# Performance work log

Hardware: AMD Instinct MI355X
Metric: run time of the kernel (lower is better)

The kernel has to match this reference:

```python
import jax, jax.numpy as jnp
import numpy as np

N_NODES = 10000
N_RAND_EDGES = 320000
IN_DIM = 256
HIDDEN = 64
HEADS = 8
OUT_DIM = 256
NEG_SLOPE = 0.2


def setup_inputs() -> dict:
    key = jax.random.key(0)
    ks = jax.random.split(key, 9)
    h = jax.random.normal(ks[0], (N_NODES, IN_DIM), dtype=jnp.float32)
    # random edges + self-loops so every dst has >=1 incoming edge
    src = jnp.concatenate([
        jax.random.randint(ks[1], (N_RAND_EDGES,), 0, N_NODES, dtype=jnp.int32),
        jnp.arange(N_NODES, dtype=jnp.int32)])
    dst = jnp.concatenate([
        jax.random.randint(ks[2], (N_RAND_EDGES,), 0, N_NODES, dtype=jnp.int32),
        jnp.arange(N_NODES, dtype=jnp.int32)])
    def glorot(k, shape):
        fan = shape[0] + shape[-1]
        s = jnp.sqrt(2.0 / fan).astype(jnp.float32)
        return jax.random.normal(k, shape, dtype=jnp.float32) * s
    W1 = glorot(ks[3], (IN_DIM, HEADS * HIDDEN))
    attn_l1 = glorot(ks[4], (HEADS, HIDDEN))
    attn_r1 = glorot(ks[5], (HEADS, HIDDEN))
    W2 = glorot(ks[6], (HEADS * HIDDEN, OUT_DIM))
    attn_l2 = glorot(ks[7], (1, OUT_DIM))
    attn_r2 = glorot(ks[8], (1, OUT_DIM))
    return {"h": h, "W1": W1, "attn_l1": attn_l1, "attn_r1": attn_r1,
            "W2": W2, "attn_l2": attn_l2, "attn_r2": attn_r2,
            "src": src, "dst": dst}


def gat_conv(x, W, attn_l, attn_r, src, dst, n_nodes):
    # x: [N, F_in]; W: [F_in, H*D]; attn_l/attn_r: [H, D]
    H, D = attn_l.shape
    feat = (x @ W).reshape(n_nodes, H, D)          # [N, H, D]
    el = jnp.einsum('nhd,hd->nh', feat, attn_l)    # [N, H]
    er = jnp.einsum('nhd,hd->nh', feat, attn_r)
    e = jax.nn.leaky_relu(el[src] + er[dst], NEG_SLOPE)  # [E, H]
    # edge softmax over incoming edges of each destination node
    m = jax.ops.segment_max(e, dst, num_segments=n_nodes)      # [N, H]
    ex = jnp.exp(e - m[dst])                                   # [E, H]
    denom = jax.ops.segment_sum(ex, dst, num_segments=n_nodes) # [N, H]
    alpha = ex / denom[dst]                                    # [E, H]
    out = jax.ops.segment_sum(alpha[:, :, None] * feat[src], dst,
                              num_segments=n_nodes)            # [N, H, D]
    return out.reshape(n_nodes, H * D)


def reference(h, W1, attn_l1, attn_r1, W2, attn_l2, attn_r2, src, dst):
    n = h.shape[0]
    x = gat_conv(h, W1, attn_l1, attn_r1, src, dst, n)   # [N, H*hidden]
    x = jax.nn.elu(x)
    out = gat_conv(x, W2, attn_l2, attn_r2, src, dst, n) # [N, out_dim]
    return out
```

## Files before the change

### kernel.cpp

```cpp
#include <hip/hip_runtime.h>
#include <hip/hip_bf16.h>

#define N_NODES 10000
#define IN_DIM 256
#define HID 512
#define HEADS 8
#define OUT_DIM 256
#define NEG 0.2f
#define CAP 128
#define WT_BLOCKS 64

typedef __hip_bfloat16 bf16;
typedef __attribute__((ext_vector_type(8))) short short8;
typedef __attribute__((ext_vector_type(4))) float f32x4;

__device__ __forceinline__ float ldm(const void* p, long i, int mode){
  if(mode) return ((const float*)p)[i];
  return __bfloat162float(((const bf16*)p)[i]);
}
__device__ __forceinline__ unsigned short f2bf(float f){
  bf16 b = __float2bfloat16(f);
  return *(unsigned short*)&b;
}
__device__ __forceinline__ float bflo(unsigned int u){ return __uint_as_float(u<<16); }
__device__ __forceinline__ float bfhi(unsigned int u){ return __uint_as_float(u&0xffff0000u); }

__global__ void detect_zero_k(const unsigned short* w1raw, int* mode, int* cnt,
                              float* el2, float* er2){
  int t = threadIdx.x;
  if(blockIdx.x==0){
    __shared__ int sbad;
    if(t==0) sbad=0;
    __syncthreads();
    int bad=0;
    for(int i=t;i<512;i+=256){
      unsigned int u = ((unsigned int)w1raw[i])<<16;
      float f = __uint_as_float(u);
      if(!(f==f) || fabsf(f) > 100.0f) bad++;
    }
    #pragma unroll
    for(int o=32;o>0;o>>=1) bad += __shfl_down(bad,o);
    if((t&63)==0) atomicAdd(&sbad, bad);
    __syncthreads();
    if(t==0) *mode = (sbad>10) ? 1 : 0;
  } else {
    int i = (blockIdx.x-1)*256 + t;
    if(i<N_NODES){ cnt[i]=0; el2[i]=0.f; er2[i]=0.f; }
  }
}

__global__ void prep2_k(const void* W1, const void* W2, unsigned short* wt1,
                        unsigned short* wt2, const int* modep,
                        const int* src, const int* dst, int* cnt, int* bucket, int E){
  int b = blockIdx.x, t = threadIdx.x;
  if(b < WT_BLOCKS){
    int md = *modep;
    __shared__ __align__(16) unsigned short tl[64*72];
    int isW2 = (b>=32);
    int bb = isW2 ? b-32 : b;
    const void* W = isW2 ? W2 : W1;
    unsigned short* wt = isW2 ? wt2 : wt1;
    int K = isW2 ? HID : IN_DIM;
    int N = isW2 ? OUT_DIM : HID;
    int sh = isW2 ? 2 : 3;
    int kt = bb >> sh, nt = bb & ((1<<sh)-1);
    int r = t>>2, c0 = (t&3)<<4;
    long srow = (long)(kt*64 + r)*N + nt*64 + c0;
    unsigned short v[16] __attribute__((aligned(16)));
    if(md){
      const float* Wf = (const float*)W;
      #pragma unroll
      for(int j=0;j<16;j+=4){
        float4 xv = *(const float4*)(Wf + srow + j);
        v[j]=f2bf(xv.x); v[j+1]=f2bf(xv.y); v[j+2]=f2bf(xv.z); v[j+3]=f2bf(xv.w);
      }
    } else {
      const unsigned short* Wb = (const unsigned short*)W;
      *(short8*)&v[0] = *(const short8*)(Wb+srow);
      *(short8*)&v[8] = *(const short8*)(Wb+srow+8);
    }
    #pragma unroll
    for(int j=0;j<16;j++) tl[(c0+j)*72 + r] = v[j];
    __syncthreads();
    int nn = t>>2, k0 = (t&3)<<4;
    short8 o0 = *(short8*)&tl[nn*72+k0];
    short8 o1 = *(short8*)&tl[nn*72+k0+8];
    long drow = (long)(nt*64+nn)*K + kt*64 + k0;
    *(short8*)(wt+drow)   = o0;
    *(short8*)(wt+drow+8) = o1;
  } else {
    int e = (b-WT_BLOCKS)*256 + t;
    if(e<E){
      int d = dst[e];
      int pos = atomicAdd(&cnt[d], 1);
      if(pos < CAP) bucket[(long)d*CAP + pos] = src[e];
    }
  }
}

__global__ __launch_bounds__(256) void gemm_k(const void* A, const unsigned short* Bt,
                                              unsigned short* C, int M, int N, int K,
                                              int asel, const int* modep,
                                              const void* al, const void* ar,
                                              float* el, float* er, int dmode){
  int md = *modep;
  int am = asel ? md : 0;
  __shared__ short As[64*40];
  __shared__ short Bs[64*40];
  __shared__ float led[64], ler[64];
  int t = threadIdx.x;
  int lane = t & 63, wave = t >> 6;
  int l15 = lane & 15, quad = lane >> 4;
  int wm = (wave>>1)*32, wn = (wave&1)*32;
  int mbase = blockIdx.y*64, nbase = blockIdx.x*64;

  f32x4 acc[2][2];
  #pragma unroll
  for(int i=0;i<2;i++)
    #pragma unroll
    for(int j=0;j<2;j++) acc[i][j] = (f32x4){0.f,0.f,0.f,0.f};

  int row = t>>2, kk = (t&3)*8;
  long arow = (long)(mbase+row)*K, brow = (long)(nbase+row)*K;
  bool av = (mbase+row) < M;
  const unsigned short* Ab = (const unsigned short*)A;
  const float* Af = (const float*)A;

  for(int k0=0;k0<K;k0+=32){
    short8 a = (short8){0,0,0,0,0,0,0,0};
    if(am){
      if(av){
        float4 x = *(const float4*)(Af + arow + k0 + kk);
        float4 y = *(const float4*)(Af + arow + k0 + kk + 4);
        a[0]=f2bf(x.x); a[1]=f2bf(x.y); a[2]=f2bf(x.z); a[3]=f2bf(x.w);
        a[4]=f2bf(y.x); a[5]=f2bf(y.y); a[6]=f2bf(y.z); a[7]=f2bf(y.w);
      }
    } else {
      if(av) a = *(const short8*)(Ab + arow + k0 + kk);
    }
    short8 b = *(const short8*)(Bt + brow + k0 + kk);
    __syncthreads();
    *(short8*)(As + row*40 + kk) = a;
    *(short8*)(Bs + row*40 + kk) = b;
    __syncthreads();
    short8 af[2], bfr[2];
    #pragma unroll
    for(int mi=0;mi<2;mi++) af[mi]  = *(short8*)(As + (wm + mi*16 + l15)*40 + quad*8);
    #pragma unroll
    for(int ni=0;ni<2;ni++) bfr[ni] = *(short8*)(Bs + (wn + ni*16 + l15)*40 + quad*8);
    #pragma unroll
    for(int mi=0;mi<2;mi++)
      #pragma unroll
      for(int ni=0;ni<2;ni++)
        acc[mi][ni] = __builtin_amdgcn_mfma_f32_16x16x32_bf16(af[mi], bfr[ni], acc[mi][ni], 0,0,0);
  }

  #pragma unroll
  for(int mi=0;mi<2;mi++){
    #pragma unroll
    for(int ni=0;ni<2;ni++){
      int grow0 = mbase + wm + mi*16 + quad*4;
      int gcol  = nbase + wn + ni*16 + l15;
      #pragma unroll
      for(int r=0;r<4;r++){
        int grow = grow0 + r;
        if(grow < M) C[(long)grow*N + gcol] = f2bf(acc[mi][ni][r]);
      }
    }
  }

  float avv[2], rvv[2];
  #pragma unroll
  for(int ni=0;ni<2;ni++){
    int gc = nbase + wn + ni*16 + l15;
    avv[ni] = ldm(al, gc, md);
    rvv[ni] = ldm(ar, gc, md);
  }
  __syncthreads();
  if(t<64){ led[t]=0.f; ler[t]=0.f; }
  __syncthreads();
  #pragma unroll
  for(int mi=0;mi<2;mi++){
    #pragma unroll
    for(int r=0;r<4;r++){
      float pl = acc[mi][0][r]*avv[0] + acc[mi][1][r]*avv[1];
      float pr = acc[mi][0][r]*rvv[0] + acc[mi][1][r]*rvv[1];
      #pragma unroll
      for(int o=1;o<16;o<<=1){ pl += __shfl_xor(pl,o); pr += __shfl_xor(pr,o); }
      if(l15==0){
        int lr = wm + mi*16 + quad*4 + r;
        atomicAdd(&led[lr], pl);
        atomicAdd(&ler[lr], pr);
      }
    }
  }
  __syncthreads();
  if(t<64){
    int grow = mbase + t;
    if(grow < M){
      if(dmode==1){
        el[(long)grow*HEADS + blockIdx.x] = led[t];
        er[(long)grow*HEADS + blockIdx.x] = ler[t];
      } else {
        atomicAdd(&el[grow], led[t]);
        atomicAdd(&er[grow], ler[t]);
      }
    }
  }
}

__global__ __launch_bounds__(128) void agg1_k(const unsigned short* fb, const float* el,
                       const float* er, const int* cnt, const int* bucket, unsigned short* x){
  int n = blockIdx.x;
  int t = threadIdx.x;
  long off = (long)n*CAP;
  int deg = cnt[n]; if(deg>CAP) deg=CAP;
  __shared__ int sidx[CAP];
  __shared__ __align__(16) float swl[CAP*8];
  __shared__ float pws[2][8];
  __shared__ float sinv[8];
  __shared__ __align__(16) float pacc[64][8];
  for(int i=t;i<deg;i+=128) sidx[i]=bucket[off+i];
  __syncthreads();
  const float* erp = er + (long)n*HEADS;
  float4 era = *(const float4*)erp, erb = *(const float4*)(erp+4);
  float err8[8] = {era.x,era.y,era.z,era.w,erb.x,erb.y,erb.z,erb.w};
  float pw[8];
  #pragma unroll
  for(int j=0;j<8;j++) pw[j]=0.f;
  for(int i=t;i<deg;i+=128){
    int s = sidx[i];
    const float* ep = el + (long)s*HEADS;
    float4 ea = *(const float4*)ep, eb = *(const float4*)(ep+4);
    float ev[8] = {ea.x,ea.y,ea.z,ea.w,eb.x,eb.y,eb.z,eb.w};
    float wv[8];
    #pragma unroll
    for(int j=0;j<8;j++){
      float e = ev[j] + err8[j];
      e = e>0.f ? e : NEG*e;
      float w = __expf(e);
      wv[j]=w; pw[j]+=w;
    }
    *(float4*)&swl[i*8]   = make_float4(wv[0],wv[1],wv[2],wv[3]);
    *(float4*)&swl[i*8+4] = make_float4(wv[4],wv[5],wv[6],wv[7]);
  }
  #pragma unroll
  for(int o=32;o>0;o>>=1)
    #pragma unroll
    for(int j=0;j<8;j++) pw[j]+=__shfl_xor(pw[j],o);
  int wv_ = t>>6, l = t&63;
  if(l==0){
    #pragma unroll
    for(int j=0;j<8;j++) pws[wv_][j]=pw[j];
  }
  __syncthreads();
  if(t<8){ float s2 = pws[0][t]+pws[1][t]; sinv[t] = s2>0.f ? 1.f/s2 : 0.f; }
  __syncthreads();
  int h = l>>3;
  int c0 = 8*l;
  float a0=0.f,a1=0.f,a2=0.f,a3=0.f,a4=0.f,a5=0.f,a6=0.f,a7=0.f;
  #pragma unroll 4
  for(int i=wv_; i<deg; i+=2){
    int s = sidx[i];
    float w = swl[i*8+h];
    uint4 u = *(const uint4*)(fb + (long)s*HID + c0);
    a0 += w*bflo(u.x); a1 += w*bfhi(u.x);
    a2 += w*bflo(u.y); a3 += w*bfhi(u.y);
    a4 += w*bflo(u.z); a5 += w*bfhi(u.z);
    a6 += w*bflo(u.w); a7 += w*bfhi(u.w);
  }
  if(wv_==1){
    *(float4*)&pacc[l][0] = make_float4(a0,a1,a2,a3);
    *(float4*)&pacc[l][4] = make_float4(a4,a5,a6,a7);
  }
  __syncthreads();
  if(wv_==0){
    float4 q0 = *(float4*)&pacc[l][0], q1 = *(float4*)&pacc[l][4];
    a0+=q0.x; a1+=q0.y; a2+=q0.z; a3+=q0.w;
    a4+=q1.x; a5+=q1.y; a6+=q1.z; a7+=q1.w;
    float inv = sinv[h];
    a0*=inv; a1*=inv; a2*=inv; a3*=inv; a4*=inv; a5*=inv; a6*=inv; a7*=inv;
    a0 = a0>0.f ? a0 : __expf(a0)-1.f;
    a1 = a1>0.f ? a1 : __expf(a1)-1.f;
    a2 = a2>0.f ? a2 : __expf(a2)-1.f;
    a3 = a3>0.f ? a3 : __expf(a3)-1.f;
    a4 = a4>0.f ? a4 : __expf(a4)-1.f;
    a5 = a5>0.f ? a5 : __expf(a5)-1.f;
    a6 = a6>0.f ? a6 : __expf(a6)-1.f;
    a7 = a7>0.f ? a7 : __expf(a7)-1.f;
    uint4 o4;
    o4.x = (unsigned int)f2bf(a0) | ((unsigned int)f2bf(a1)<<16);
    o4.y = (unsigned int)f2bf(a2) | ((unsigned int)f2bf(a3)<<16);
    o4.z = (unsigned int)f2bf(a4) | ((unsigned int)f2bf(a5)<<16);
    o4.w = (unsigned int)f2bf(a6) | ((unsigned int)f2bf(a7)<<16);
    *(uint4*)(x + (long)n*HID + c0) = o4;
  }
}

__global__ __launch_bounds__(64) void agg2_k(const unsigned short* fb, const float* el,
                       const float* er, const int* cnt, const int* bucket, void* out,
                       const int* modep){
  int md = *modep;
  int n = blockIdx.x, t = threadIdx.x;
  long off = (long)n*CAP;
  int deg = cnt[n]; if(deg>CAP) deg=CAP;
  __shared__ int sidx[CAP];
  __shared__ float wl[CAP];
  for(int i=t;i<deg;i+=64) sidx[i]=bucket[off+i];
  __syncthreads();
  float ern = er[n];
  float pw = 0.f;
  for(int i=t;i<deg;i+=64){
    int s = sidx[i];
    float e = el[s]+ern; e = e>0.f ? e : NEG*e;
    float w = __expf(e);
    wl[i]=w;
    pw += w;
  }
  #pragma unroll
  for(int o=32;o>0;o>>=1) pw += __shfl_xor(pw,o);
  float inv = pw>0.f ? 1.f/pw : 0.f;
  __syncthreads();
  int half = t>>5, l = t&31;
  int c0 = 8*l;
  float a0=0.f,a1=0.f,a2=0.f,a3=0.f,a4=0.f,a5=0.f,a6=0.f,a7=0.f;
  #pragma unroll 4
  for(int i=half; i<deg; i+=2){
    int s = sidx[i];
    float w = wl[i];
    uint4 u = *(const uint4*)(fb + (long)s*OUT_DIM + c0);
    a0 += w*bflo(u.x); a1 += w*bfhi(u.x);
    a2 += w*bflo(u.y); a3 += w*bfhi(u.y);
    a4 += w*bflo(u.z); a5 += w*bfhi(u.z);
    a6 += w*bflo(u.w); a7 += w*bfhi(u.w);
  }
  a0 += __shfl_xor(a0,32); a1 += __shfl_xor(a1,32);
  a2 += __shfl_xor(a2,32); a3 += __shfl_xor(a3,32);
  a4 += __shfl_xor(a4,32); a5 += __shfl_xor(a5,32);
  a6 += __shfl_xor(a6,32); a7 += __shfl_xor(a7,32);
  if(half==0){
    a0*=inv; a1*=inv; a2*=inv; a3*=inv; a4*=inv; a5*=inv; a6*=inv; a7*=inv;
    long oi = (long)n*OUT_DIM + c0;
    if(md){
      float* of = (float*)out;
      *(float4*)(of+oi)   = make_float4(a0,a1,a2,a3);
      *(float4*)(of+oi+4) = make_float4(a4,a5,a6,a7);
    } else {
      unsigned short* ob = (unsigned short*)out;
      uint4 o4;
      o4.x = (unsigned int)f2bf(a0) | ((unsigned int)f2bf(a1)<<16);
      o4.y = (unsigned int)f2bf(a2) | ((unsigned int)f2bf(a3)<<16);
      o4.z = (unsigned int)f2bf(a4) | ((unsigned int)f2bf(a5)<<16);
      o4.w = (unsigned int)f2bf(a6) | ((unsigned int)f2bf(a7)<<16);
      *(uint4*)(ob+oi) = o4;
    }
  }
}

extern "C" void kernel_launch(void* const* d_in, const int* in_sizes, int n_in,
                              void* d_out, int out_size, void* d_ws, size_t ws_size,
                              hipStream_t stream){
  (void)n_in; (void)out_size; (void)ws_size;
  const void* h_in = d_in[0];
  const void* W1   = d_in[1];
  const void* al1  = d_in[2];
  const void* ar1  = d_in[3];
  const void* W2   = d_in[4];
  const void* al2  = d_in[5];
  const void* ar2  = d_in[6];
  const int* src = (const int*)d_in[7];
  const int* dst = (const int*)d_in[8];
  int E = in_sizes[7];

  char* ws = (char*)d_ws;
  size_t o = 0;
  auto alloc = [&](size_t b){ size_t c=o; o += (b+255)&~(size_t)255; return c; };
  unsigned short* f1b  = (unsigned short*)(ws + alloc((size_t)N_NODES*HID*2));
  unsigned short* f2b  = (unsigned short*)(ws + alloc((size_t)N_NODES*OUT_DIM*2));
  unsigned short* xbuf = (unsigned short*)(ws + alloc((size_t)N_NODES*HID*2));
  unsigned short* wt1  = (unsigned short*)(ws + alloc((size_t)IN_DIM*HID*2));
  unsigned short* wt2  = (unsigned short*)(ws + alloc((size_t)HID*OUT_DIM*2));
  float* el1   = (float*)(ws + alloc((size_t)N_NODES*HEADS*4));
  float* er1   = (float*)(ws + alloc((size_t)N_NODES*HEADS*4));
  float* el2   = (float*)(ws + alloc((size_t)N_NODES*4));
  float* er2   = (float*)(ws + alloc((size_t)N_NODES*4));
  int* cnt     = (int*)(ws + alloc((size_t)N_NODES*4));
  int* bucket  = (int*)(ws + alloc((size_t)N_NODES*CAP*4));
  int* modep   = (int*)(ws + alloc(256));

  detect_zero_k<<<1+(N_NODES+255)/256,256,0,stream>>>(
      (const unsigned short*)W1, modep, cnt, el2, er2);
  prep2_k<<<WT_BLOCKS+(E+255)/256,256,0,stream>>>(
      W1, W2, wt1, wt2, modep, src, dst, cnt, bucket, E);

  gemm_k<<<dim3(HID/64,(N_NODES+63)/64),256,0,stream>>>(
      h_in, wt1, f1b, N_NODES, HID, IN_DIM, 1, modep, al1, ar1, el1, er1, 1);
  agg1_k<<<N_NODES,128,0,stream>>>(f1b, el1, er1, cnt, bucket, xbuf);

  gemm_k<<<dim3(OUT_DIM/64,(N_NODES+63)/64),256,0,stream>>>(
      xbuf, wt2, f2b, N_NODES, OUT_DIM, HID, 0, modep, al2, ar2, el2, er2, 2);
  agg2_k<<<N_NODES,64,0,stream>>>(f2b, el2, er2, cnt, bucket, d_out, modep);
}
```

Measured before the change: 186.4 us.

## Merge prep kernels, fold edge bucketing into GEMM launch, double-buffer GEMM K loop

Combines mode detection, zeroing and weight transposition into one kernel, with each transpose block recomputing the dtype mode locally instead of waiting on a separate launch. Edge bucketing moves into extra blocks of the first GEMM launch so it runs alongside the matmul. The GEMM K-step grows from 32 to 64, and next-tile global loads are register-prefetched before the LDS stores. The aim is fewer launches and better latency hiding, at the cost of more registers and LDS per block and some redundant detection work.

```diff
diff --git a/kernel.cpp b/kernel.cpp
--- a/kernel.cpp
+++ b/kernel.cpp
@@ -8,7 +8,8 @@
 #define OUT_DIM 256
 #define NEG 0.2f
 #define CAP 128
-#define WT_BLOCKS 64
+#define ZB 40
+#define TB 64
 
 typedef __hip_bfloat16 bf16;
 typedef __attribute__((ext_vector_type(8))) short short8;
@@ -25,10 +26,11 @@
 __device__ __forceinline__ float bflo(unsigned int u){ return __uint_as_float(u<<16); }
 __device__ __forceinline__ float bfhi(unsigned int u){ return __uint_as_float(u&0xffff0000u); }
 
-__global__ void detect_zero_k(const unsigned short* w1raw, int* mode, int* cnt,
-                              float* el2, float* er2){
-  int t = threadIdx.x;
-  if(blockIdx.x==0){
+__global__ void prep_all_k(const unsigned short* w1raw, const void* W1, const void* W2,
+                           unsigned short* wt1, unsigned short* wt2, int* modep,
+                           int* cnt, float* el2, float* er2){
+  int b = blockIdx.x, t = threadIdx.x;
+  if(b==0){
     __shared__ int sbad;
     if(t==0) sbad=0;
     __syncthreads();
@@ -42,77 +44,93 @@
     for(int o=32;o>0;o>>=1) bad += __shfl_down(bad,o);
     if((t&63)==0) atomicAdd(&sbad, bad);
     __syncthreads();
-    if(t==0) *mode = (sbad>10) ? 1 : 0;
+    if(t==0) *modep = (sbad>10) ? 1 : 0;
+    return;
+  }
+  if(b < 1+ZB){
+    int i = (b-1)*256 + t;
+    if(i<N_NODES){ cnt[i]=0; el2[i]=0.f; er2[i]=0.f; }
+    return;
+  }
+  __shared__ int sbad;
+  __shared__ __align__(16) unsigned short tl[64*72];
+  if(t==0) sbad=0;
+  __syncthreads();
+  int bad=0;
+  for(int i=t;i<512;i+=256){
+    unsigned int u = ((unsigned int)w1raw[i])<<16;
+    float f = __uint_as_float(u);
+    if(!(f==f) || fabsf(f) > 100.0f) bad++;
+  }
+  #pragma unroll
+  for(int o=32;o>0;o>>=1) bad += __shfl_down(bad,o);
+  if((t&63)==0) atomicAdd(&sbad, bad);
+  __syncthreads();
+  int md = sbad>10;
+  int bb0 = b - (1+ZB);
+  int isW2 = (bb0>=32);
+  int bb = isW2 ? bb0-32 : bb0;
+  const void* W = isW2 ? W2 : W1;
+  unsigned short* wt = isW2 ? wt2 : wt1;
+  int K = isW2 ? HID : IN_DIM;
+  int N = isW2 ? OUT_DIM : HID;
+  int sh = isW2 ? 2 : 3;
+  int kt = bb >> sh, nt = bb & ((1<<sh)-1);
+  int r = t>>2, c0 = (t&3)<<4;
+  long srow = (long)(kt*64 + r)*N + nt*64 + c0;
+  unsigned short v[16] __attribute__((aligned(16)));
+  if(md){
+    const float* Wf = (const float*)W;
+    #pragma unroll
+    for(int j=0;j<16;j+=4){
+      float4 xv = *(const float4*)(Wf + srow + j);
+      v[j]=f2bf(xv.x); v[j+1]=f2bf(xv.y); v[j+2]=f2bf(xv.z); v[j+3]=f2bf(xv.w);
+    }
   } else {
-    int i = (blockIdx.x-1)*256 + t;
-    if(i<N_NODES){ cnt[i]=0; el2[i]=0.f; er2[i]=0.f; }
-  }
-}
-
-__global__ void prep2_k(const void* W1, const void* W2, unsigned short* wt1,
-                        unsigned short* wt2, const int* modep,
-                        const int* src, const int* dst, int* cnt, int* bucket, int E){
-  int b = blockIdx.x, t = threadIdx.x;
-  if(b < WT_BLOCKS){
-    int md = *modep;
-    __shared__ __align__(16) unsigned short tl[64*72];
-    int isW2 = (b>=32);
-    int bb = isW2 ? b-32 : b;
-    const void* W = isW2 ? W2 : W1;
-    unsigned short* wt = isW2 ? wt2 : wt1;
-    int K = isW2 ? HID : IN_DIM;
-    int N = isW2 ? OUT_DIM : HID;
-    int sh = isW2 ? 2 : 3;
-    int kt = bb >> sh, nt = bb & ((1<<sh)-1);
-    int r = t>>2, c0 = (t&3)<<4;
-    long srow = (long)(kt*64 + r)*N + nt*64 + c0;
-    unsigned short v[16] __attribute__((aligned(16)));
-    if(md){
-      const float* Wf = (const float*)W;
-      #pragma unroll
-      for(int j=0;j<16;j+=4){
-        float4 xv = *(const float4*)(Wf + srow + j);
-        v[j]=f2bf(xv.x); v[j+1]=f2bf(xv.y); v[j+2]=f2bf(xv.z); v[j+3]=f2bf(xv.w);
-      }
-    } else {
-      const unsigned short* Wb = (const unsigned short*)W;
-      *(short8*)&v[0] = *(const short8*)(Wb+srow);
-      *(short8*)&v[8] = *(const short8*)(Wb+srow+8);
-    }
-    #pragma unroll
-    for(int j=0;j<16;j++) tl[(c0+j)*72 + r] = v[j];
-    __syncthreads();
-    int nn = t>>2, k0 = (t&3)<<4;
-    short8 o0 = *(short8*)&tl[nn*72+k0];
-    short8 o1 = *(short8*)&tl[nn*72+k0+8];
-    long drow = (long)(nt*64+nn)*K + kt*64 + k0;
-    *(short8*)(wt+drow)   = o0;
-    *(short8*)(wt+drow+8) = o1;
-  } else {
-    int e = (b-WT_BLOCKS)*256 + t;
+    const unsigned short* Wb = (const unsigned short*)W;
+    *(short8*)&v[0] = *(const short8*)(Wb+srow);
+    *(short8*)&v[8] = *(const short8*)(Wb+srow+8);
+  }
+  #pragma unroll
+  for(int j=0;j<16;j++) tl[(c0+j)*72 + r] = v[j];
+  __syncthreads();
+  int nn = t>>2, k0 = (t&3)<<4;
+  short8 o0 = *(short8*)&tl[nn*72+k0];
+  short8 o1 = *(short8*)&tl[nn*72+k0+8];
+  long drow = (long)(nt*64+nn)*K + kt*64 + k0;
+  *(short8*)(wt+drow)   = o0;
+  *(short8*)(wt+drow+8) = o1;
+}
+
+__global__ __launch_bounds__(256) void gemm_k(const void* A, const unsigned short* Bt,
+                                              unsigned short* C, int M, int N, int K,
+                                              int asel, const int* modep,
+                                              const void* al, const void* ar,
+                                              float* el, float* er, int dmode,
+                                              const int* src, const int* dst,
+                                              int* cnt, int* bucket, int E,
+                                              int gemmBlocks, int nbx){
+  int blk = blockIdx.x;
+  if(blk >= gemmBlocks){
+    int e = (blk-gemmBlocks)*256 + threadIdx.x;
     if(e<E){
       int d = dst[e];
       int pos = atomicAdd(&cnt[d], 1);
       if(pos < CAP) bucket[(long)d*CAP + pos] = src[e];
     }
-  }
-}
-
-__global__ __launch_bounds__(256) void gemm_k(const void* A, const unsigned short* Bt,
-                                              unsigned short* C, int M, int N, int K,
-                                              int asel, const int* modep,
-                                              const void* al, const void* ar,
-                                              float* el, float* er, int dmode){
+    return;
+  }
   int md = *modep;
   int am = asel ? md : 0;
-  __shared__ short As[64*40];
-  __shared__ short Bs[64*40];
+  __shared__ short As[64*72];
+  __shared__ short Bs[64*72];
   __shared__ float led[64], ler[64];
   int t = threadIdx.x;
   int lane = t & 63, wave = t >> 6;
   int l15 = lane & 15, quad = lane >> 4;
   int wm = (wave>>1)*32, wn = (wave&1)*32;
-  int mbase = blockIdx.y*64, nbase = blockIdx.x*64;
+  int bx = blk % nbx, by = blk / nbx;
+  int mbase = by*64, nbase = bx*64;
 
   f32x4 acc[2][2];
   #pragma unroll
@@ -120,39 +138,70 @@
     #pragma unroll
     for(int j=0;j<2;j++) acc[i][j] = (f32x4){0.f,0.f,0.f,0.f};
 
-  int row = t>>2, kk = (t&3)*8;
+  int row = t>>2, kk = (t&3)*16;
   long arow = (long)(mbase+row)*K, brow = (long)(nbase+row)*K;
   bool av = (mbase+row) < M;
   const unsigned short* Ab = (const unsigned short*)A;
   const float* Af = (const float*)A;
 
-  for(int k0=0;k0<K;k0+=32){
-    short8 a = (short8){0,0,0,0,0,0,0,0};
+  short8 a0,a1,b0,b1, na0,na1,nb0,nb1;
+  a0=a1=b0=b1 = (short8){0,0,0,0,0,0,0,0};
+  na0=na1=nb0=nb1 = (short8){0,0,0,0,0,0,0,0};
+
+  {
+    long ao = arow + kk;
     if(am){
       if(av){
-        float4 x = *(const float4*)(Af + arow + k0 + kk);
-        float4 y = *(const float4*)(Af + arow + k0 + kk + 4);
-        a[0]=f2bf(x.x); a[1]=f2bf(x.y); a[2]=f2bf(x.z); a[3]=f2bf(x.w);
-        a[4]=f2bf(y.x); a[5]=f2bf(y.y); a[6]=f2bf(y.z); a[7]=f2bf(y.w);
+        float4 x0 = *(const float4*)(Af+ao),   x1 = *(const float4*)(Af+ao+4);
+        float4 x2 = *(const float4*)(Af+ao+8), x3 = *(const float4*)(Af+ao+12);
+        a0[0]=f2bf(x0.x);a0[1]=f2bf(x0.y);a0[2]=f2bf(x0.z);a0[3]=f2bf(x0.w);
+        a0[4]=f2bf(x1.x);a0[5]=f2bf(x1.y);a0[6]=f2bf(x1.z);a0[7]=f2bf(x1.w);
+        a1[0]=f2bf(x2.x);a1[1]=f2bf(x2.y);a1[2]=f2bf(x2.z);a1[3]=f2bf(x2.w);
+        a1[4]=f2bf(x3.x);a1[5]=f2bf(x3.y);a1[6]=f2bf(x3.z);a1[7]=f2bf(x3.w);
       }
-    } else {
-      if(av) a = *(const short8*)(Ab + arow + k0 + kk);
-    }
-    short8 b = *(const short8*)(Bt + brow + k0 + kk);
+    } else if(av){
+      a0 = *(const short8*)(Ab+ao); a1 = *(const short8*)(Ab+ao+8);
+    }
+    b0 = *(const short8*)(Bt+brow+kk); b1 = *(const short8*)(Bt+brow+kk+8);
+  }
+
+  for(int k0=0;k0<K;k0+=64){
+    if(k0+64 < K){
+      long ao = arow + k0 + 64 + kk;
+      if(am){
+        if(av){
+          float4 x0 = *(const float4*)(Af+ao),   x1 = *(const float4*)(Af+ao+4);
+          float4 x2 = *(const float4*)(Af+ao+8), x3 = *(const float4*)(Af+ao+12);
+          na0[0]=f2bf(x0.x);na0[1]=f2bf(x0.y);na0[2]=f2bf(x0.z);na0[3]=f2bf(x0.w);
+          na0[4]=f2bf(x1.x);na0[5]=f2bf(x1.y);na0[6]=f2bf(x1.z);na0[7]=f2bf(x1.w);
+          na1[0]=f2bf(x2.x);na1[1]=f2bf(x2.y);na1[2]=f2bf(x2.z);na1[3]=f2bf(x2.w);
+          na1[4]=f2bf(x3.x);na1[5]=f2bf(x3.y);na1[6]=f2bf(x3.z);na1[7]=f2bf(x3.w);
+        }
+      } else if(av){
+        na0 = *(const short8*)(Ab+ao); na1 = *(const short8*)(Ab+ao+8);
+      }
+      nb0 = *(const short8*)(Bt+brow+k0+64+kk); nb1 = *(const short8*)(Bt+brow+k0+64+kk+8);
+    }
     __syncthreads();
-    *(short8*)(As + row*40 + kk) = a;
-    *(short8*)(Bs + row*40 + kk) = b;
+    *(short8*)(As + row*72 + kk)   = a0;
+    *(short8*)(As + row*72 + kk+8) = a1;
+    *(short8*)(Bs + row*72 + kk)   = b0;
+    *(short8*)(Bs + row*72 + kk+8) = b1;
     __syncthreads();
-    short8 af[2], bfr[2];
-    #pragma unroll
-    for(int mi=0;mi<2;mi++) af[mi]  = *(short8*)(As + (wm + mi*16 + l15)*40 + quad*8);
-    #pragma unroll
-    for(int ni=0;ni<2;ni++) bfr[ni] = *(short8*)(Bs + (wn + ni*16 + l15)*40 + quad*8);
-    #pragma unroll
-    for(int mi=0;mi<2;mi++)
+    #pragma unroll
+    for(int ks=0;ks<2;ks++){
+      short8 af[2], bfr[2];
       #pragma unroll
-      for(int ni=0;ni<2;ni++)
-        acc[mi][ni] = __builtin_amdgcn_mfma_f32_16x16x32_bf16(af[mi], bfr[ni], acc[mi][ni], 0,0,0);
+      for(int mi=0;mi<2;mi++) af[mi]  = *(short8*)(As + (wm + mi*16 + l15)*72 + ks*32 + quad*8);
+      #pragma unroll
+      for(int ni=0;ni<2;ni++) bfr[ni] = *(short8*)(Bs + (wn + ni*16 + l15)*72 + ks*32 + quad*8);
+      #pragma unroll
+      for(int mi=0;mi<2;mi++)
+        #pragma unroll
+        for(int ni=0;ni<2;ni++)
+          acc[mi][ni] = __builtin_amdgcn_mfma_f32_16x16x32_bf16(af[mi], bfr[ni], acc[mi][ni], 0,0,0);
+    }
+    a0=na0; a1=na1; b0=nb0; b1=nb1;
   }
 
   #pragma unroll
@@ -199,8 +248,8 @@
     int grow = mbase + t;
     if(grow < M){
       if(dmode==1){
-        el[(long)grow*HEADS + blockIdx.x] = led[t];
-        er[(long)grow*HEADS + blockIdx.x] = ler[t];
+        el[(long)grow*HEADS + bx] = led[t];
+        er[(long)grow*HEADS + bx] = ler[t];
       } else {
         atomicAdd(&el[grow], led[t]);
         atomicAdd(&er[grow], ler[t]);
@@ -388,16 +437,21 @@
   int* bucket  = (int*)(ws + alloc((size_t)N_NODES*CAP*4));
   int* modep   = (int*)(ws + alloc(256));
 
-  detect_zero_k<<<1+(N_NODES+255)/256,256,0,stream>>>(
-      (const unsigned short*)W1, modep, cnt, el2, er2);
-  prep2_k<<<WT_BLOCKS+(E+255)/256,256,0,stream>>>(
-      W1, W2, wt1, wt2, modep, src, dst, cnt, bucket, E);
-
-  gemm_k<<<dim3(HID/64,(N_NODES+63)/64),256,0,stream>>>(
-      h_in, wt1, f1b, N_NODES, HID, IN_DIM, 1, modep, al1, ar1, el1, er1, 1);
+  prep_all_k<<<1+ZB+TB,256,0,stream>>>(
+      (const unsigned short*)W1, W1, W2, wt1, wt2, modep, cnt, el2, er2);
+
+  int gb1 = (HID/64)*((N_NODES+63)/64);
+  int sb  = (E+255)/256;
+  gemm_k<<<gb1+sb,256,0,stream>>>(
+      h_in, wt1, f1b, N_NODES, HID, IN_DIM, 1, modep, al1, ar1, el1, er1, 1,
+      src, dst, cnt, bucket, E, gb1, HID/64);
+
   agg1_k<<<N_NODES,128,0,stream>>>(f1b, el1, er1, cnt, bucket, xbuf);
 
-  gemm_k<<<dim3(OUT_DIM/64,(N_NODES+63)/64),256,0,stream>>>(
-      xbuf, wt2, f2b, N_NODES, OUT_DIM, HID, 0, modep, al2, ar2, el2, er2, 2);
+  int gb2 = (OUT_DIM/64)*((N_NODES+63)/64);
+  gemm_k<<<gb2,256,0,stream>>>(
+      xbuf, wt2, f2b, N_NODES, OUT_DIM, HID, 0, modep, al2, ar2, el2, er2, 2,
+      src, dst, cnt, bucket, 0, gb2, OUT_DIM/64);
+
   agg2_k<<<N_NODES,64,0,stream>>>(f2b, el2, er2, cnt, bucket, d_out, modep);
 }
```

New measurement: 175.8 us. -5.7%, faster.
